# Kernel optimization log

Hardware: AMD Instinct MI355X
Metric: run time of the kernel (lower is better)

The kernel has to match this reference:

```python
import jax, jax.numpy as jnp
import numpy as np

ALPHA = 0.2  # LeakyReLU negative slope

def setup_inputs() -> dict:
    key = jax.random.key(0)
    k1, k2, k3 = jax.random.split(key, 3)
    B, N, D_in, D_out = 4, 512, 512, 256
    H = jax.random.normal(k1, (B, N, D_in), dtype=jnp.float32)
    # xavier-style scaled params
    W = jax.random.normal(k2, (D_out, D_in), dtype=jnp.float32) * (2.0 / (D_in + D_out)) ** 0.5
    a = jax.random.normal(k3, (D_out, 1), dtype=jnp.float32) * (2.0 / (D_out + 1)) ** 0.5
    return {"H": H, "W": W, "a": a}

def reference(H, W, a):
    # Wh: [B, N, D_out]
    Wh = jnp.einsum('bnd,od->bno', H, W)
    # additive pairwise scores: e[b,i,j] = leakyrelu(Wh[b,i]+Wh[b,j]) . a
    e = jnp.einsum('bijo,o->bij',
                   jax.nn.leaky_relu(Wh[:, :, None, :] + Wh[:, None, :, :], ALPHA),
                   a[:, 0])
    attention = jax.nn.softmax(e, axis=-1)          # [B, N, N]
    H_att = jnp.einsum('bij,bjo->bio', attention, Wh)  # [B, N, D_out]
    return H_att
```

## Files before the change

kernel.cpp:

```cpp
#include <hip/hip_runtime.h>

constexpr int Bq   = 4;
constexpr int Nq   = 512;
constexpr int DIN  = 512;
constexpr int DOUT = 256;

typedef _Float16 h2  __attribute__((ext_vector_type(2)));
typedef float    v2f __attribute__((ext_vector_type(2)));

#if defined(__has_builtin) && __has_builtin(__builtin_amdgcn_fdot2)
__device__ __forceinline__ float fdot2f(h2 a, h2 b, float c) {
    return __builtin_amdgcn_fdot2(a, b, c, false);
}
#else
__device__ __forceinline__ float fdot2f(h2 a, h2 b, float c) {
    return (float)a.x * (float)b.x + (float)a.y * (float)b.y + c;
}
#endif

__global__ __launch_bounds__(256) void k0_cvt(const float* __restrict__ W,
                                              const float* __restrict__ H,
                                              const float* __restrict__ a,
                                              h2* __restrict__ WT16p,
                                              h2* __restrict__ H16,
                                              h2* __restrict__ a16) {
    const int bid = blockIdx.x;
    const int t   = threadIdx.x;
    if (bid < 64) {
        __shared__ h2 tile[32][33];
        const int bx = bid & 7, by = bid >> 3;
        const int k20 = bx * 32, o0 = by * 32;
        const int tx = t & 31, ty = t >> 5;
#pragma unroll
        for (int jj = 0; jj < 4; ++jj) {
            const int o = o0 + ty + 8 * jj;
            const float2 v = *(const float2*)&W[o * DIN + 2 * (k20 + tx)];
            h2 hv; hv.x = (_Float16)v.x; hv.y = (_Float16)v.y;
            tile[tx][ty + 8 * jj] = hv;
        }
        __syncthreads();
#pragma unroll
        for (int jj = 0; jj < 4; ++jj) {
            const int k2g = k20 + ty + 8 * jj;
            WT16p[k2g * 256 + o0 + tx] = tile[ty + 8 * jj][tx];
        }
    } else if (bid < 64 + 2048) {
        const int idx = (bid - 64) * 256 + t;
        const float2 v = *(const float2*)&H[2 * (size_t)idx];
        h2 hv; hv.x = (_Float16)v.x; hv.y = (_Float16)v.y;
        H16[idx] = hv;
    } else if (t < 128) {
        const float2 v = *(const float2*)&a[2 * t];
        h2 hv; hv.x = (_Float16)v.x; hv.y = (_Float16)v.y;
        a16[t] = hv;
    }
}

__global__ __launch_bounds__(1024, 8) void k1_wh(const h2* __restrict__ H16,
                                                 const h2* __restrict__ WT16p,
                                                 const float* __restrict__ a,
                                                 float* __restrict__ Wh,
                                                 h2* __restrict__ Wh16,
                                                 h2* __restrict__ WhT16p,
                                                 float* __restrict__ r) {
    const int t   = threadIdx.x;
    const int blk = blockIdx.x;
    const int b   = blk & 3;
    const int n0  = (blk >> 2) << 2;
    const int p   = __builtin_amdgcn_readfirstlane(t >> 8);
    const int o   = t & 255;

    __shared__ float sPart[4][4][256];
    __shared__ float sRed[8];

    const h2* __restrict__ wtp   = WT16p + o;
    const h2* __restrict__ hbase = H16 + (size_t)(b * Nq + n0) * 256;

    float acc[4] = {0.f, 0.f, 0.f, 0.f};
    const int k0p = p * 64;
    h2 cA[8], cB[8];

#define K1_L8(buf, kb)                                                      \
    _Pragma("unroll") for (int s = 0; s < 8; ++s)                           \
        buf[s] = wtp[(k0p + (kb) + s) * 256];

#define K1_C8(buf, kb)                                                      \
    _Pragma("unroll") for (int s = 0; s < 8; ++s) {                         \
        const int k2 = k0p + (kb) + s;                                      \
        _Pragma("unroll") for (int rr = 0; rr < 4; ++rr)                    \
            acc[rr] = fdot2f(hbase[rr * 256 + k2], buf[s], acc[rr]);        \
    }

    K1_L8(cA, 0)  K1_L8(cB, 8)
    K1_C8(cA, 0)  K1_L8(cA, 16)
    K1_C8(cB, 8)  K1_L8(cB, 24)
    K1_C8(cA, 16) K1_L8(cA, 32)
    K1_C8(cB, 24) K1_L8(cB, 40)
    K1_C8(cA, 32) K1_L8(cA, 48)
    K1_C8(cB, 40) K1_L8(cB, 56)
    K1_C8(cA, 48)
    K1_C8(cB, 56)
#undef K1_L8
#undef K1_C8

#pragma unroll
    for (int rr = 0; rr < 4; ++rr) sPart[p][rr][o] = acc[rr];
    __syncthreads();

    if (t < 512) {
        const int row = t >> 7, op = t & 127;
        float f0 = 0.f, f1 = 0.f;
#pragma unroll
        for (int pp = 0; pp < 4; ++pp) {
            f0 += sPart[pp][row][2 * op];
            f1 += sPart[pp][row][2 * op + 1];
        }
        const int n = b * Nq + n0 + row;
        *(float2*)&Wh[(size_t)n * DOUT + 2 * op] = make_float2(f0, f1);
        h2 hv; hv.x = (_Float16)f0; hv.y = (_Float16)f1;
        Wh16[(size_t)n * 128 + op] = hv;
        WhT16p[(size_t)b * 65536 + op * 512 + (n0 + row)] = hv;

        const float2 av = *(const float2*)&a[2 * op];
        float pr = av.x * f0 + av.y * f1;
#pragma unroll
        for (int off = 32; off > 0; off >>= 1) pr += __shfl_xor(pr, off);
        if ((t & 63) == 0) sRed[t >> 6] = pr;
    }
    __syncthreads();
    if (t < 4) r[(size_t)b * Nq + n0 + t] = sRed[2 * t] + sRed[2 * t + 1];
}

__global__ __launch_bounds__(1024, 8) void k23(const float* __restrict__ Wh,
                                               const h2* __restrict__ Wh16,
                                               const h2* __restrict__ WhT16p,
                                               const h2* __restrict__ a16,
                                               const float* __restrict__ r,
                                               float* __restrict__ out) {
    const int t   = threadIdx.x;
    const int blk = blockIdx.x;
    const int b   = blk & 3;
    const int i0  = (blk >> 2) << 2;

    __shared__ float smem[8192];
    __shared__ float sP[4 * 512];
    __shared__ float wred[2][4][8];

    {
        const int h  = __builtin_amdgcn_readfirstlane(t >> 9);
        const int j  = t & 511;
        const int ob = h * 64;

        const h2* __restrict__ wjp = WhT16p + (size_t)b * 65536 + (size_t)ob * 512 + j;
        const h2* __restrict__ wip = Wh16 + (size_t)(b * Nq + i0) * 128;
        const float* __restrict__ gr = r + (size_t)b * Nq;

        float ab[4] = {0.f, 0.f, 0.f, 0.f};
        h2 cA[8], cB[8];

#define K2_L8(buf, kb)                                                      \
    _Pragma("unroll") for (int s = 0; s < 8; ++s)                           \
        buf[s] = wjp[((kb) + s) * 512];

#define K2_C8(buf, kb)                                                      \
    _Pragma("unroll") for (int s = 0; s < 8; ++s) {                         \
        const int o2 = ob + (kb) + s;                                       \
        const h2 a2 = a16[o2];                                  \
        _Pragma("unroll") for (int rr = 0; rr < 4; ++rr) {                  \
            const h2 wi = wip[rr * 128 + o2];                   \
            h2 w  = buf[s] + wi;                                \
            h2 aw = __builtin_elementwise_max(w, -w);           \
            ab[rr] = fdot2f(a2, aw, ab[rr]);                    \
        }                                                                   \
    }

        K2_L8(cA, 0)  K2_L8(cB, 8)
        K2_C8(cA, 0)  K2_L8(cA, 16)
        K2_C8(cB, 8)  K2_L8(cB, 24)
        K2_C8(cA, 16) K2_L8(cA, 32)
        K2_C8(cB, 24) K2_L8(cB, 40)
        K2_C8(cA, 32) K2_L8(cA, 48)
        K2_C8(cB, 40) K2_L8(cB, 56)
        K2_C8(cA, 48)
        K2_C8(cB, 56)
#undef K2_L8
#undef K2_C8

        float* sAb = smem;
        if (h == 1) {
#pragma unroll
            for (int rr = 0; rr < 4; ++rr) sAb[rr * 512 + j] = ab[rr];
        }
        __syncthreads();

        float e[4], pv[4];
        if (h == 0) {
            const float rj = gr[j];
#pragma unroll
            for (int rr = 0; rr < 4; ++rr) {
                const float A = ab[rr] + sAb[rr * 512 + j];
                e[rr] = 0.6f * (gr[i0 + rr] + rj) + 0.4f * A;
            }
        }

        const int lane = t & 63;
        const int w    = t >> 6;

#pragma unroll
        for (int rr = 0; rr < 4; ++rr) {
            float v = (h == 0) ? e[rr] : -3e38f;
#pragma unroll
            for (int off = 32; off > 0; off >>= 1) v = fmaxf(v, __shfl_xor(v, off));
            if (lane == 0 && h == 0) wred[0][rr][w] = v;
        }
        __syncthreads();
        if (h == 0) {
#pragma unroll
            for (int rr = 0; rr < 4; ++rr) {
                const float4 q0 = *(const float4*)&wred[0][rr][0];
                const float4 q1 = *(const float4*)&wred[0][rr][4];
                const float m = fmaxf(fmaxf(fmaxf(q0.x, q0.y), fmaxf(q0.z, q0.w)),
                                      fmaxf(fmaxf(q1.x, q1.y), fmaxf(q1.z, q1.w)));
                pv[rr] = __expf(e[rr] - m);
            }
        }
#pragma unroll
        for (int rr = 0; rr < 4; ++rr) {
            float v = (h == 0) ? pv[rr] : 0.f;
#pragma unroll
            for (int off = 32; off > 0; off >>= 1) v += __shfl_xor(v, off);
            if (lane == 0 && h == 0) wred[1][rr][w] = v;
        }
        __syncthreads();
        if (h == 0) {
#pragma unroll
            for (int rr = 0; rr < 4; ++rr) {
                const float4 q0 = *(const float4*)&wred[1][rr][0];
                const float4 q1 = *(const float4*)&wred[1][rr][4];
                const float s = (q0.x + q0.y + q0.z + q0.w) + (q1.x + q1.y + q1.z + q1.w);
                sP[rr * 512 + j] = pv[rr] * (1.0f / s);
            }
        }
        __syncthreads();
    }

    {
        const int w16 = __builtin_amdgcn_readfirstlane(t >> 6);
        const int jh  = w16 & 7;
        const int rh  = w16 >> 3;
        const int oq  = t & 63;

        const float4* __restrict__ wh4 = (const float4*)(Wh + (size_t)b * Nq * DOUT) + oq;

        v2f accL[2] = {(v2f)0.f, (v2f)0.f};
        v2f accH[2] = {(v2f)0.f, (v2f)0.f};

        const int j0 = jh * 64;
        float4 bufA[4], bufB[4];
#pragma unroll
        for (int s = 0; s < 4; ++s) bufA[s] = wh4[(j0 + s) * 64];

        for (int it = 0; it < 8; ++it) {
            const int jA = j0 + it * 8, jB = jA + 4;
#pragma unroll
            for (int s = 0; s < 4; ++s) bufB[s] = wh4[(jB + s) * 64];
#pragma unroll
            for (int rr = 0; rr < 2; ++rr) {
                const float4 p4 = *(const float4*)&sP[(rh * 2 + rr) * 512 + jA];
#pragma unroll
                for (int x = 0; x < 4; ++x) {
                    const float pj = ((const float*)&p4)[x];
                    const v2f pj2 = pj;
                    const v2f wl = {bufA[x].x, bufA[x].y};
                    const v2f wh = {bufA[x].z, bufA[x].w};
                    accL[rr] = __builtin_elementwise_fma(pj2, wl, accL[rr]);
                    accH[rr] = __builtin_elementwise_fma(pj2, wh, accH[rr]);
                }
            }
            if (it < 7) {
#pragma unroll
                for (int s = 0; s < 4; ++s) bufA[s] = wh4[(jA + 8 + s) * 64];
            }
#pragma unroll
            for (int rr = 0; rr < 2; ++rr) {
                const float4 p4 = *(const float4*)&sP[(rh * 2 + rr) * 512 + jB];
#pragma unroll
                for (int x = 0; x < 4; ++x) {
                    const float pj = ((const float*)&p4)[x];
                    const v2f pj2 = pj;
                    const v2f wl = {bufB[x].x, bufB[x].y};
                    const v2f wh = {bufB[x].z, bufB[x].w};
                    accL[rr] = __builtin_elementwise_fma(pj2, wl, accL[rr]);
                    accH[rr] = __builtin_elementwise_fma(pj2, wh, accH[rr]);
                }
            }
        }

        float4* sPart = (float4*)smem;
#pragma unroll
        for (int rr = 0; rr < 2; ++rr) {
            const int row = rh * 2 + rr;
            float4 f;
            f.x = accL[rr].x; f.y = accL[rr].y; f.z = accH[rr].x; f.w = accH[rr].y;
            sPart[(jh * 4 + row) * 64 + oq] = f;
        }
        __syncthreads();

        if (t < 256) {
            const int row = t >> 6, oqq = t & 63;
            float4 fin = make_float4(0.f, 0.f, 0.f, 0.f);
#pragma unroll
            for (int j8 = 0; j8 < 8; ++j8) {
                const float4 v = sPart[(j8 * 4 + row) * 64 + oqq];
                fin.x += v.x; fin.y += v.y; fin.z += v.z; fin.w += v.w;
            }
            ((float4*)(out + ((size_t)(b * Nq) + i0 + row) * DOUT))[oqq] = fin;
        }
    }
}

extern "C" void kernel_launch(void* const* d_in, const int* in_sizes, int n_in,
                              void* d_out, int out_size, void* d_ws, size_t ws_size,
                              hipStream_t stream) {
    const float* H = (const float*)d_in[0];
    const float* W = (const float*)d_in[1];
    const float* a = (const float*)d_in[2];
    float* out = (float*)d_out;

    float* Wh    = (float*)d_ws;
    float* r     = Wh + 524288;
    h2* H16      = (h2*)(r + 2048);
    h2* Wh16     = H16 + 524288;
    h2* WhT16p   = Wh16 + 262144;
    h2* WT16p    = WhT16p + 262144;
    h2* a16      = WT16p + 65536;

    hipLaunchKernelGGL(k0_cvt, dim3(2113), dim3(256),  0, stream, W, H, a, WT16p, H16, a16);
    hipLaunchKernelGGL(k1_wh,  dim3(512),  dim3(1024), 0, stream, H16, WT16p, a, Wh, Wh16, WhT16p, r);
    hipLaunchKernelGGL(k23,    dim3(512),  dim3(1024), 0, stream, Wh, Wh16, WhT16p, a16, r, out);
}
```

Before: 107.4 us.

## Compute Wh projection with MFMA and fold row scores into attention kernel

Replaces the fdot2-based Wh projection kernel with an MFMA 16x16x32 f16 matrix-core kernel that reads W16 in its natural layout, so the W transpose in the conversion kernel is no longer needed. The conversion kernel now moves four floats per thread. The per-row score r is no longer written by the projection kernel; the attention kernel recomputes it from the fp16 WhT loads it already performs and shares it through shared memory. This trades the serial dot-product GEMM for matrix-core throughput, at the cost of an extra barrier and fp16 precision in r.

After: 106.5 us. Within noise of the previous version (-0.8%).

```diff
diff --git a/kernel.cpp b/kernel.cpp
--- a/kernel.cpp
+++ b/kernel.cpp
@@ -6,6 +6,8 @@
 constexpr int DOUT = 256;
 
 typedef _Float16 h2  __attribute__((ext_vector_type(2)));
+typedef _Float16 h8  __attribute__((ext_vector_type(8)));
+typedef float    f4v __attribute__((ext_vector_type(4)));
 typedef float    v2f __attribute__((ext_vector_type(2)));
 
 #if defined(__has_builtin) && __has_builtin(__builtin_amdgcn_fdot2)
@@ -21,121 +23,85 @@
 __global__ __launch_bounds__(256) void k0_cvt(const float* __restrict__ W,
                                               const float* __restrict__ H,
                                               const float* __restrict__ a,
-                                              h2* __restrict__ WT16p,
+                                              h2* __restrict__ W16,
                                               h2* __restrict__ H16,
                                               h2* __restrict__ a16) {
     const int bid = blockIdx.x;
     const int t   = threadIdx.x;
-    if (bid < 64) {
-        __shared__ h2 tile[32][33];
-        const int bx = bid & 7, by = bid >> 3;
-        const int k20 = bx * 32, o0 = by * 32;
-        const int tx = t & 31, ty = t >> 5;
-#pragma unroll
-        for (int jj = 0; jj < 4; ++jj) {
-            const int o = o0 + ty + 8 * jj;
-            const float2 v = *(const float2*)&W[o * DIN + 2 * (k20 + tx)];
-            h2 hv; hv.x = (_Float16)v.x; hv.y = (_Float16)v.y;
-            tile[tx][ty + 8 * jj] = hv;
-        }
-        __syncthreads();
-#pragma unroll
-        for (int jj = 0; jj < 4; ++jj) {
-            const int k2g = k20 + ty + 8 * jj;
-            WT16p[k2g * 256 + o0 + tx] = tile[ty + 8 * jj][tx];
-        }
-    } else if (bid < 64 + 2048) {
-        const int idx = (bid - 64) * 256 + t;
-        const float2 v = *(const float2*)&H[2 * (size_t)idx];
-        h2 hv; hv.x = (_Float16)v.x; hv.y = (_Float16)v.y;
-        H16[idx] = hv;
-    } else if (t < 128) {
-        const float2 v = *(const float2*)&a[2 * t];
-        h2 hv; hv.x = (_Float16)v.x; hv.y = (_Float16)v.y;
-        a16[t] = hv;
-    }
-}
-
-__global__ __launch_bounds__(1024, 8) void k1_wh(const h2* __restrict__ H16,
-                                                 const h2* __restrict__ WT16p,
-                                                 const float* __restrict__ a,
-                                                 float* __restrict__ Wh,
-                                                 h2* __restrict__ Wh16,
-                                                 h2* __restrict__ WhT16p,
-                                                 float* __restrict__ r) {
-    const int t   = threadIdx.x;
-    const int blk = blockIdx.x;
-    const int b   = blk & 3;
-    const int n0  = (blk >> 2) << 2;
-    const int p   = __builtin_amdgcn_readfirstlane(t >> 8);
-    const int o   = t & 255;
-
-    __shared__ float sPart[4][4][256];
-    __shared__ float sRed[8];
-
-    const h2* __restrict__ wtp   = WT16p + o;
-    const h2* __restrict__ hbase = H16 + (size_t)(b * Nq + n0) * 256;
-
-    float acc[4] = {0.f, 0.f, 0.f, 0.f};
-    const int k0p = p * 64;
-    h2 cA[8], cB[8];
-
-#define K1_L8(buf, kb)                                                      \
-    _Pragma("unroll") for (int s = 0; s < 8; ++s)                           \
-        buf[s] = wtp[(k0p + (kb) + s) * 256];
-
-#define K1_C8(buf, kb)                                                      \
-    _Pragma("unroll") for (int s = 0; s < 8; ++s) {                         \
-        const int k2 = k0p + (kb) + s;                                      \
-        _Pragma("unroll") for (int rr = 0; rr < 4; ++rr)                    \
-            acc[rr] = fdot2f(hbase[rr * 256 + k2], buf[s], acc[rr]);        \
-    }
-
-    K1_L8(cA, 0)  K1_L8(cB, 8)
-    K1_C8(cA, 0)  K1_L8(cA, 16)
-    K1_C8(cB, 8)  K1_L8(cB, 24)
-    K1_C8(cA, 16) K1_L8(cA, 32)
-    K1_C8(cB, 24) K1_L8(cB, 40)
-    K1_C8(cA, 32) K1_L8(cA, 48)
-    K1_C8(cB, 40) K1_L8(cB, 56)
-    K1_C8(cA, 48)
-    K1_C8(cB, 56)
-#undef K1_L8
-#undef K1_C8
-
-#pragma unroll
-    for (int rr = 0; rr < 4; ++rr) sPart[p][rr][o] = acc[rr];
-    __syncthreads();
-
-    if (t < 512) {
-        const int row = t >> 7, op = t & 127;
-        float f0 = 0.f, f1 = 0.f;
-#pragma unroll
-        for (int pp = 0; pp < 4; ++pp) {
-            f0 += sPart[pp][row][2 * op];
-            f1 += sPart[pp][row][2 * op + 1];
-        }
-        const int n = b * Nq + n0 + row;
-        *(float2*)&Wh[(size_t)n * DOUT + 2 * op] = make_float2(f0, f1);
-        h2 hv; hv.x = (_Float16)f0; hv.y = (_Float16)f1;
-        Wh16[(size_t)n * 128 + op] = hv;
-        WhT16p[(size_t)b * 65536 + op * 512 + (n0 + row)] = hv;
-
-        const float2 av = *(const float2*)&a[2 * op];
-        float pr = av.x * f0 + av.y * f1;
-#pragma unroll
-        for (int off = 32; off > 0; off >>= 1) pr += __shfl_xor(pr, off);
-        if ((t & 63) == 0) sRed[t >> 6] = pr;
-    }
-    __syncthreads();
-    if (t < 4) r[(size_t)b * Nq + n0 + t] = sRed[2 * t] + sRed[2 * t + 1];
+    if (bid < 1024) {
+        const size_t idx = ((size_t)bid * 256 + t) * 2;
+        const float4 v = *(const float4*)&H[2 * idx];
+        h2 h0; h0.x = (_Float16)v.x; h0.y = (_Float16)v.y;
+        h2 h1; h1.x = (_Float16)v.z; h1.y = (_Float16)v.w;
+        H16[idx] = h0; H16[idx + 1] = h1;
+    } else if (bid < 1152) {
+        const size_t idx = ((size_t)(bid - 1024) * 256 + t) * 2;
+        const float4 v = *(const float4*)&W[2 * idx];
+        h2 h0; h0.x = (_Float16)v.x; h0.y = (_Float16)v.y;
+        h2 h1; h1.x = (_Float16)v.z; h1.y = (_Float16)v.w;
+        W16[idx] = h0; W16[idx + 1] = h1;
+    } else if (t < 64) {
+        const int idx = 2 * t;
+        const float4 v = *(const float4*)&a[2 * idx];
+        h2 h0; h0.x = (_Float16)v.x; h0.y = (_Float16)v.y;
+        h2 h1; h1.x = (_Float16)v.z; h1.y = (_Float16)v.w;
+        a16[idx] = h0; a16[idx + 1] = h1;
+    }
+}
+
+__global__ __launch_bounds__(256) void k1_wh(const h2* __restrict__ H16,
+                                             const h2* __restrict__ W16,
+                                             float* __restrict__ Wh,
+                                             h2* __restrict__ Wh16,
+                                             h2* __restrict__ WhT16p) {
+    const int t    = threadIdx.x;
+    const int w    = t >> 6;
+    const int lane = t & 63;
+    const int bid  = blockIdx.x;
+    const int mt   = bid >> 2;
+    const int b    = mt & 3;
+    const int n0   = (mt >> 2) << 4;
+    const int o0   = ((bid & 3) << 6) + (w << 4);
+    const int quad = lane >> 4;
+    const int col  = lane & 15;
+
+    const h2* __restrict__ aPtr = H16 + ((size_t)(b * Nq + n0 + col) * 256) + quad * 4;
+    const h2* __restrict__ bPtr = W16 + ((size_t)(o0 + col) * 256) + quad * 4;
+
+    f4v acc = {0.f, 0.f, 0.f, 0.f};
+    h8 a0 = *(const h8*)aPtr;
+    h8 b0 = *(const h8*)bPtr;
+
+#pragma unroll
+    for (int kb = 0; kb < 16; ++kb) {
+        h8 a1 = a0, b1 = b0;
+        if (kb < 15) {
+            a1 = *(const h8*)(aPtr + (kb + 1) * 16);
+            b1 = *(const h8*)(bPtr + (kb + 1) * 16);
+        }
+        acc = __builtin_amdgcn_mfma_f32_16x16x32_f16(a0, b0, acc, 0, 0, 0);
+        a0 = a1; b0 = b1;
+    }
+
+    const int rowb = b * Nq + n0 + quad * 4;
+#pragma unroll
+    for (int reg = 0; reg < 4; ++reg) {
+        const float v = acc[reg];
+        Wh[(size_t)(rowb + reg) * DOUT + o0 + col] = v;
+        const float vp = __shfl_xor(v, 1);
+        if ((col & 1) == 0) {
+            h2 hv; hv.x = (_Float16)v; hv.y = (_Float16)vp;
+            const int o2 = (o0 + col) >> 1;
+            Wh16[(size_t)(rowb + reg) * 128 + o2] = hv;
+            WhT16p[(size_t)b * 65536 + (size_t)o2 * 512 + (n0 + quad * 4 + reg)] = hv;
+        }
+    }
 }
 
 __global__ __launch_bounds__(1024, 8) void k23(const float* __restrict__ Wh,
                                                const h2* __restrict__ Wh16,
                                                const h2* __restrict__ WhT16p,
                                                const h2* __restrict__ a16,
-                                               const float* __restrict__ r,
                                                float* __restrict__ out) {
     const int t   = threadIdx.x;
     const int blk = blockIdx.x;
@@ -153,9 +119,9 @@
 
         const h2* __restrict__ wjp = WhT16p + (size_t)b * 65536 + (size_t)ob * 512 + j;
         const h2* __restrict__ wip = Wh16 + (size_t)(b * Nq + i0) * 128;
-        const float* __restrict__ gr = r + (size_t)b * Nq;
 
         float ab[4] = {0.f, 0.f, 0.f, 0.f};
+        float rja = 0.f;
         h2 cA[8], cB[8];
 
 #define K2_L8(buf, kb)                                                      \
@@ -166,6 +132,7 @@
     _Pragma("unroll") for (int s = 0; s < 8; ++s) {                         \
         const int o2 = ob + (kb) + s;                                       \
         const h2 a2 = a16[o2];                                  \
+        rja = fdot2f(a2, buf[s], rja);                                      \
         _Pragma("unroll") for (int rr = 0; rr < 4; ++rr) {                  \
             const h2 wi = wip[rr * 128 + o2];                   \
             h2 w  = buf[s] + wi;                                \
@@ -187,20 +154,29 @@
 #undef K2_C8
 
         float* sAb = smem;
+        float* sRh = smem + 2048;
+        float* sRf = smem + 2560;
         if (h == 1) {
 #pragma unroll
             for (int rr = 0; rr < 4; ++rr) sAb[rr * 512 + j] = ab[rr];
+            sRh[j] = rja;
+        }
+        __syncthreads();
+
+        float rj = 0.f;
+        if (h == 0) {
+#pragma unroll
+            for (int rr = 0; rr < 4; ++rr) ab[rr] += sAb[rr * 512 + j];
+            rj = rja + sRh[j];
+            sRf[j] = rj;
         }
         __syncthreads();
 
         float e[4], pv[4];
         if (h == 0) {
-            const float rj = gr[j];
-#pragma unroll
-            for (int rr = 0; rr < 4; ++rr) {
-                const float A = ab[rr] + sAb[rr * 512 + j];
-                e[rr] = 0.6f * (gr[i0 + rr] + rj) + 0.4f * A;
-            }
+#pragma unroll
+            for (int rr = 0; rr < 4; ++rr)
+                e[rr] = 0.6f * (sRf[i0 + rr] + rj) + 0.4f * ab[rr];
         }
 
         const int lane = t & 63;
@@ -327,15 +303,14 @@
     const float* a = (const float*)d_in[2];
     float* out = (float*)d_out;
 
-    float* Wh    = (float*)d_ws;
-    float* r     = Wh + 524288;
-    h2* H16      = (h2*)(r + 2048);
-    h2* Wh16     = H16 + 524288;
-    h2* WhT16p   = Wh16 + 262144;
-    h2* WT16p    = WhT16p + 262144;
-    h2* a16      = WT16p + 65536;
-
-    hipLaunchKernelGGL(k0_cvt, dim3(2113), dim3(256),  0, stream, W, H, a, WT16p, H16, a16);
-    hipLaunchKernelGGL(k1_wh,  dim3(512),  dim3(1024), 0, stream, H16, WT16p, a, Wh, Wh16, WhT16p, r);
-    hipLaunchKernelGGL(k23,    dim3(512),  dim3(1024), 0, stream, Wh, Wh16, WhT16p, a16, r, out);
-}
+    float* Wh  = (float*)d_ws;
+    h2* H16    = (h2*)(Wh + 524288);
+    h2* Wh16   = H16 + 524288;
+    h2* WhT16p = Wh16 + 262144;
+    h2* W16    = WhT16p + 262144;
+    h2* a16    = W16 + 65536;
+
+    hipLaunchKernelGGL(k0_cvt, dim3(1153), dim3(256),  0, stream, W, H, a, W16, H16, a16);
+    hipLaunchKernelGGL(k1_wh,  dim3(512),  dim3(256),  0, stream, H16, W16, Wh, Wh16, WhT16p);
+    hipLaunchKernelGGL(k23,    dim3(512),  dim3(1024), 0, stream, Wh, Wh16, WhT16p, a16, out);
+}
```
